# Kernel tuning notes

Measured on AMD Instinct MI355X. Metric: run time of the kernel, lower is better.

The kernel has to match this reference:

```python
import math
import jax, jax.numpy as jnp
import numpy as np

H, DK = 16, 64            # n_heads, d_kv
NUM_BUCKETS, MAX_DIST = 32, 128


def _relative_position_buckets(S):
    # Bidirectional (encoder) T5 bucketization of relative positions.
    ctx = jnp.arange(S, dtype=jnp.int32)[:, None]      # query positions
    mem = jnp.arange(S, dtype=jnp.int32)[None, :]      # key positions
    rp = mem - ctx                                     # [S, S]
    nb = NUM_BUCKETS // 2
    rb = (rp > 0).astype(jnp.int32) * nb
    n = jnp.abs(rp)
    max_exact = nb // 2
    is_small = n < max_exact
    large = max_exact + (
        jnp.log(jnp.maximum(n, 1).astype(jnp.float32) / max_exact)
        / math.log(MAX_DIST / max_exact)
        * (nb - max_exact)
    ).astype(jnp.int32)
    large = jnp.minimum(large, nb - 1)
    return rb + jnp.where(is_small, n, large)          # [S, S] int32


def setup_inputs() -> dict:
    key = jax.random.key(0)
    ks = jax.random.split(key, 6)
    B, S, D = 4, 1024, 1024
    inner = H * DK
    std = 0.02
    return {
        "hidden_states": jax.random.normal(ks[0], (B, S, D), jnp.float32),
        "Wq": jax.random.normal(ks[1], (inner, D), jnp.float32) * std,
        "Wk": jax.random.normal(ks[2], (inner, D), jnp.float32) * std,
        "Wv": jax.random.normal(ks[3], (inner, D), jnp.float32) * std,
        "Wo": jax.random.normal(ks[4], (D, inner), jnp.float32) * std,
        "rel_bias": jax.random.normal(ks[5], (NUM_BUCKETS, H), jnp.float32) * std,
    }


def reference(hidden_states, Wq, Wk, Wv, Wo, rel_bias):
    B, S, D = hidden_states.shape

    def proj(W):  # bias-free linear + split heads -> [B, H, S, DK]
        return (hidden_states @ W.T).reshape(B, S, H, DK).transpose(0, 2, 1, 3)

    q, k, v = proj(Wq), proj(Wk), proj(Wv)
    # T5: NO 1/sqrt(d) scaling
    scores = jnp.einsum("bhqd,bhkd->bhqk", q, k)       # [B, H, S, S]
    bias = rel_bias[_relative_position_buckets(S)]     # [S, S, H]
    scores = scores + bias.transpose(2, 0, 1)[None]    # broadcast over batch
    attn = jax.nn.softmax(scores, axis=-1)
    ctx = jnp.einsum("bhqk,bhkd->bhqd", attn, v)       # [B, H, S, DK]
    ctx = ctx.transpose(0, 2, 1, 3).reshape(B, S, H * DK)
    return ctx @ Wo.T                                  # [B, S, D]
```

## Files before the change

### kernel.cpp

```cpp
#include <hip/hip_runtime.h>

typedef _Float16 half8 __attribute__((ext_vector_type(8)));
typedef _Float16 half4_t __attribute__((ext_vector_type(4)));
typedef float f32x4 __attribute__((ext_vector_type(4)));

#define GK 1024
#define MEG (1024 * 1024)

#define GLD16(gptr, lptr) \
    __builtin_amdgcn_global_load_lds((const __attribute__((address_space(1))) void*)(gptr), \
                                     (__attribute__((address_space(3))) void*)(lptr), 16, 0, 0)

__global__ void cvt_all_kernel(const float* __restrict__ hidden,
                               const float* __restrict__ Wq,
                               const float* __restrict__ Wk,
                               const float* __restrict__ Wv,
                               const float* __restrict__ Wo,
                               _Float16* __restrict__ ws) {
    int b = blockIdx.x;
    const float* src;
    _Float16* dst;
    if (b < 4096)      { src = hidden; dst = ws; }
    else if (b < 5120) { src = Wq; dst = ws + 4 * MEG; b -= 4096; }
    else if (b < 6144) { src = Wk; dst = ws + 5 * MEG; b -= 5120; }
    else if (b < 7168) { src = Wv; dst = ws + 6 * MEG; b -= 6144; }
    else               { src = Wo; dst = ws + 7 * MEG; b -= 7168; }
    int i = (b * 256 + threadIdx.x) * 4;
    f32x4 v = *(const f32x4*)(src + i);
    half4_t h;
    h[0] = (_Float16)v[0]; h[1] = (_Float16)v[1];
    h[2] = (_Float16)v[2]; h[3] = (_Float16)v[3];
    *(half4_t*)(dst + i) = h;
}

template<int MODE>
__global__ __launch_bounds__(256) void gemm_kernel(
    const _Float16* __restrict__ A,
    const _Float16* __restrict__ B0,
    const _Float16* __restrict__ B1,
    const _Float16* __restrict__ B2,
    _Float16* __restrict__ O0,
    _Float16* __restrict__ O1,
    _Float16* __restrict__ O2,
    float* __restrict__ Of)
{
    const _Float16* Bw = B0;
    _Float16* Oh = O0;
    if (MODE == 0) {
        int z = blockIdx.z;
        Bw = (z == 0) ? B0 : ((z == 1) ? B1 : B2);
        Oh = (z == 0) ? O0 : ((z == 1) ? O1 : O2);
    }
    __shared__ __attribute__((aligned(16))) _Float16 sA[128][32];
    __shared__ __attribute__((aligned(16))) _Float16 sB[128][32];

    const int tid = threadIdx.x;
    const int wave = tid >> 6, lane = tid & 63;
    const int quad = lane >> 4, l16 = lane & 15;
    const int wr = wave >> 1, wc = wave & 1;
    const int M0 = blockIdx.y * 128, N0 = blockIdx.x * 128;

    const int rl = lane >> 2;
    const int cl = (lane & 3) * 8;
    const size_t aOff0 = (size_t)(M0 + wave * 16 + rl) * GK + cl;
    const size_t aOff1 = aOff0 + (size_t)64 * GK;
    const size_t bOff0 = (size_t)(N0 + wave * 16 + rl) * GK + cl;
    const size_t bOff1 = bOff0 + (size_t)64 * GK;
    _Float16* ldsA0 = &sA[wave * 16][0];
    _Float16* ldsA1 = &sA[64 + wave * 16][0];
    _Float16* ldsB0 = &sB[wave * 16][0];
    _Float16* ldsB1 = &sB[64 + wave * 16][0];

    f32x4 acc[4][4] = {};

    for (int kt = 0; kt < GK / 32; ++kt) {
        const int ko = kt * 32;
        GLD16(A + aOff0 + ko, ldsA0);
        GLD16(A + aOff1 + ko, ldsA1);
        GLD16(Bw + bOff0 + ko, ldsB0);
        GLD16(Bw + bOff1 + ko, ldsB1);
        __syncthreads();
        half8 af[4], bf[4];
        #pragma unroll
        for (int i = 0; i < 4; ++i)
            af[i] = *(const half8*)&sA[wr * 64 + i * 16 + l16][quad * 8];
        #pragma unroll
        for (int j = 0; j < 4; ++j)
            bf[j] = *(const half8*)&sB[wc * 64 + j * 16 + l16][quad * 8];
        #pragma unroll
        for (int i = 0; i < 4; ++i)
            #pragma unroll
            for (int j = 0; j < 4; ++j)
                acc[i][j] = __builtin_amdgcn_mfma_f32_16x16x32_f16(af[i], bf[j], acc[i][j], 0, 0, 0);
        __syncthreads();
    }

    #pragma unroll
    for (int i = 0; i < 4; ++i) {
        #pragma unroll
        for (int j = 0; j < 4; ++j) {
            #pragma unroll
            for (int r = 0; r < 4; ++r) {
                int m = M0 + wr * 64 + i * 16 + quad * 4 + r;
                int n = N0 + wc * 64 + j * 16 + l16;
                float v = acc[i][j][r];
                if (MODE == 0) {
                    int b = m >> 10, s = m & 1023, hh = n >> 6, d = n & 63;
                    Oh[((size_t)((b * 16 + hh) * 1024 + s)) * 64 + d] = (_Float16)v;
                } else {
                    Of[(size_t)m * 1024 + n] = v;
                }
            }
        }
    }
}

__global__ __launch_bounds__(256) void transpose_v_kernel(
    const _Float16* __restrict__ V, _Float16* __restrict__ VT) {
    __shared__ _Float16 tile[64][65];
    const int s0 = blockIdx.x * 64;
    const int bh = blockIdx.y;
    const _Float16* Vb = V + (size_t)bh * 1024 * 64;
    _Float16* Tb = VT + (size_t)bh * 64 * 1024;
    const int tr = threadIdx.x >> 6;
    const int tc = threadIdx.x & 63;
    #pragma unroll
    for (int i = 0; i < 16; ++i) {
        int r = i * 4 + tr;
        tile[r][tc] = Vb[(size_t)(s0 + r) * 64 + tc];
    }
    __syncthreads();
    #pragma unroll
    for (int i = 0; i < 16; ++i) {
        int d = i * 4 + tr;
        Tb[(size_t)d * 1024 + s0 + tc] = tile[tc][d];
    }
}

__global__ __launch_bounds__(256) void attn_kernel(
    const _Float16* __restrict__ Q,
    const _Float16* __restrict__ K,
    const _Float16* __restrict__ VT,
    const float* __restrict__ rel_bias,
    _Float16* __restrict__ ctx)
{
    const int S = 1024;
    const int q0 = blockIdx.x * 64;
    const int h = blockIdx.y;
    const int b = blockIdx.z;
    const int bh = b * 16 + h;
    const _Float16* Qh = Q + (size_t)bh * S * 64;
    const _Float16* Kh = K + (size_t)bh * S * 64;
    const _Float16* VTh = VT + (size_t)bh * 64 * S;

    __shared__ __attribute__((aligned(16))) _Float16 sQ[64][72];
    __shared__ __attribute__((aligned(16))) _Float16 sK[64][72];
    __shared__ __attribute__((aligned(16))) _Float16 sVt[64][72];
    __shared__ __attribute__((aligned(16))) _Float16 sP[4][16][72];
    __shared__ _Float16 sBias[1088];

    const int tid = threadIdx.x;
    const int wave = tid >> 6, lane = tid & 63;
    const int quad = lane >> 4, l16 = lane & 15;

    {
        int r = tid >> 3, c = (tid & 7) * 8;
        *(half8*)&sQ[r][c]      = *(const half8*)(Qh + (size_t)(q0 + r) * 64 + c);
        *(half8*)&sQ[r + 32][c] = *(const half8*)(Qh + (size_t)(q0 + r + 32) * 64 + c);
    }
    for (int i = tid; i < 1087; i += 256) {
        int delta = i - (q0 + 63);
        int rb = (delta > 0) ? 16 : 0;
        int n = (delta < 0) ? -delta : delta;
        int bucket;
        if (n < 8) bucket = rb + n;
        else bucket = rb + 8 + (n >= 12) + (n >= 16) + (n >= 23) + (n >= 32)
                             + (n >= 46) + (n >= 64) + (n >= 91);
        sBias[i] = (_Float16)rel_bias[bucket * 16 + h];
    }
    __syncthreads();

    half8 qf0 = *(const half8*)&sQ[wave * 16 + l16][quad * 8];
    half8 qf1 = *(const half8*)&sQ[wave * 16 + l16][32 + quad * 8];

    float m_run = -INFINITY, l_run = 0.0f;
    f32x4 acc[4] = {};

    for (int kt = 0; kt < 16; ++kt) {
        __syncthreads();
        {
            int r = tid >> 3, c = (tid & 7) * 8;
            *(half8*)&sK[r][c]      = *(const half8*)(Kh + (size_t)(kt * 64 + r) * 64 + c);
            *(half8*)&sK[r + 32][c] = *(const half8*)(Kh + (size_t)(kt * 64 + r + 32) * 64 + c);
            *(half8*)&sVt[r][c]      = *(const half8*)(VTh + (size_t)r * S + kt * 64 + c);
            *(half8*)&sVt[r + 32][c] = *(const half8*)(VTh + (size_t)(r + 32) * S + kt * 64 + c);
        }
        __syncthreads();

        f32x4 sc[4] = {};
        #pragma unroll
        for (int j = 0; j < 4; ++j) {
            half8 kf0 = *(const half8*)&sK[j * 16 + l16][quad * 8];
            half8 kf1 = *(const half8*)&sK[j * 16 + l16][32 + quad * 8];
            sc[j] = __builtin_amdgcn_mfma_f32_16x16x32_f16(kf0, qf0, sc[j], 0, 0, 0);
            sc[j] = __builtin_amdgcn_mfma_f32_16x16x32_f16(kf1, qf1, sc[j], 0, 0, 0);
        }

        const int bbase = kt * 64 + quad * 4 - wave * 16 - l16 + 63;
        #pragma unroll
        for (int j = 0; j < 4; ++j)
            #pragma unroll
            for (int r = 0; r < 4; ++r)
                sc[j][r] += (float)sBias[bbase + j * 16 + r];

        float mx = fmaxf(fmaxf(fmaxf(sc[0][0], sc[0][1]), fmaxf(sc[0][2], sc[0][3])),
                         fmaxf(fmaxf(sc[1][0], sc[1][1]), fmaxf(sc[1][2], sc[1][3])));
        mx = fmaxf(mx, fmaxf(fmaxf(fmaxf(sc[2][0], sc[2][1]), fmaxf(sc[2][2], sc[2][3])),
                             fmaxf(fmaxf(sc[3][0], sc[3][1]), fmaxf(sc[3][2], sc[3][3]))));
        mx = fmaxf(mx, __shfl_xor(mx, 16));
        mx = fmaxf(mx, __shfl_xor(mx, 32));
        float mnew = fmaxf(m_run, mx);
        float alpha = __expf(m_run - mnew);
        m_run = mnew;

        float ps = 0.0f;
        #pragma unroll
        for (int j = 0; j < 4; ++j) {
            half4_t pw;
            #pragma unroll
            for (int r = 0; r < 4; ++r) {
                float p = __expf(sc[j][r] - mnew);
                ps += p;
                pw[r] = (_Float16)p;
            }
            *(half4_t*)&sP[wave][l16][j * 16 + quad * 4] = pw;
        }
        l_run = l_run * alpha + ps;
        #pragma unroll
        for (int dt = 0; dt < 4; ++dt) acc[dt] *= alpha;
        __syncthreads();

        half8 pf0 = *(const half8*)&sP[wave][l16][quad * 8];
        half8 pf1 = *(const half8*)&sP[wave][l16][32 + quad * 8];
        #pragma unroll
        for (int dt = 0; dt < 4; ++dt) {
            half8 vf0 = *(const half8*)&sVt[dt * 16 + l16][quad * 8];
            half8 vf1 = *(const half8*)&sVt[dt * 16 + l16][32 + quad * 8];
            acc[dt] = __builtin_amdgcn_mfma_f32_16x16x32_f16(vf0, pf0, acc[dt], 0, 0, 0);
            acc[dt] = __builtin_amdgcn_mfma_f32_16x16x32_f16(vf1, pf1, acc[dt], 0, 0, 0);
        }
    }

    l_run += __shfl_xor(l_run, 16);
    l_run += __shfl_xor(l_run, 32);
    const float inv = 1.0f / l_run;
    const size_t qg = (size_t)(b * 1024 + q0 + wave * 16 + l16);
    #pragma unroll
    for (int dt = 0; dt < 4; ++dt) {
        half4_t o;
        #pragma unroll
        for (int r = 0; r < 4; ++r) o[r] = (_Float16)(acc[dt][r] * inv);
        *(half4_t*)&ctx[qg * 1024 + h * 64 + dt * 16 + quad * 4] = o;
    }
}

extern "C" void kernel_launch(void* const* d_in, const int* in_sizes, int n_in,
                              void* d_out, int out_size, void* d_ws, size_t ws_size,
                              hipStream_t stream) {
    const float* hidden   = (const float*)d_in[0];
    const float* Wq       = (const float*)d_in[1];
    const float* Wk       = (const float*)d_in[2];
    const float* Wv       = (const float*)d_in[3];
    const float* Wo       = (const float*)d_in[4];
    const float* rel_bias = (const float*)d_in[5];
    float* out = (float*)d_out;

    _Float16* ws    = (_Float16*)d_ws;
    _Float16* h16   = ws;
    _Float16* wq16  = ws + 4 * (size_t)MEG;
    _Float16* wk16  = ws + 5 * (size_t)MEG;
    _Float16* wv16  = ws + 6 * (size_t)MEG;
    _Float16* wo16  = ws + 7 * (size_t)MEG;
    _Float16* Qs    = ws + 8 * (size_t)MEG;
    _Float16* Ks    = ws + 12 * (size_t)MEG;
    _Float16* Vs    = ws + 16 * (size_t)MEG;
    _Float16* ctx16 = ws + 20 * (size_t)MEG;
    _Float16* VTs   = h16;

    cvt_all_kernel<<<8192, 256, 0, stream>>>(hidden, Wq, Wk, Wv, Wo, ws);

    gemm_kernel<0><<<dim3(8, 32, 3), 256, 0, stream>>>(
        h16, wq16, wk16, wv16, Qs, Ks, Vs, nullptr);

    transpose_v_kernel<<<dim3(16, 64), 256, 0, stream>>>(Vs, VTs);

    attn_kernel<<<dim3(16, 16, 4), 256, 0, stream>>>(Qs, Ks, VTs, rel_bias, ctx16);

    gemm_kernel<1><<<dim3(8, 32, 1), 256, 0, stream>>>(
        ctx16, wo16, nullptr, nullptr, nullptr, nullptr, nullptr, out);
}
```

Measured before the change: 217.9 us.

## Widen GEMM K-step to 64 and use constant bias for far attention tiles

The GEMM main loop now loads two 32-wide K chunks into separate LDS buffers per iteration, which halves the number of barrier pairs and issues more MFMAs between syncs. The attention kernel uses the fact that T5 relative-position buckets saturate beyond distance 128. For key tiles at least three tiles away from the query tile it adds a single bias value instead of sixteen LDS lookups. This uses more LDS in the GEMM and adds a branch in attention. The bias shortcut holds only because the bucket is constant at those distances.

```diff
diff --git a/kernel.cpp b/kernel.cpp
--- a/kernel.cpp
+++ b/kernel.cpp
@@ -51,8 +51,8 @@
         Bw = (z == 0) ? B0 : ((z == 1) ? B1 : B2);
         Oh = (z == 0) ? O0 : ((z == 1) ? O1 : O2);
     }
-    __shared__ __attribute__((aligned(16))) _Float16 sA[128][32];
-    __shared__ __attribute__((aligned(16))) _Float16 sB[128][32];
+    __shared__ __attribute__((aligned(16))) _Float16 sA[2][128][32];
+    __shared__ __attribute__((aligned(16))) _Float16 sB[2][128][32];
 
     const int tid = threadIdx.x;
     const int wave = tid >> 6, lane = tid & 63;
@@ -62,36 +62,42 @@
 
     const int rl = lane >> 2;
     const int cl = (lane & 3) * 8;
-    const size_t aOff0 = (size_t)(M0 + wave * 16 + rl) * GK + cl;
-    const size_t aOff1 = aOff0 + (size_t)64 * GK;
-    const size_t bOff0 = (size_t)(N0 + wave * 16 + rl) * GK + cl;
-    const size_t bOff1 = bOff0 + (size_t)64 * GK;
-    _Float16* ldsA0 = &sA[wave * 16][0];
-    _Float16* ldsA1 = &sA[64 + wave * 16][0];
-    _Float16* ldsB0 = &sB[wave * 16][0];
-    _Float16* ldsB1 = &sB[64 + wave * 16][0];
+    const size_t aRow0 = (size_t)(M0 + wave * 16 + rl) * GK + cl;
+    const size_t aRow1 = aRow0 + (size_t)64 * GK;
+    const size_t bRow0 = (size_t)(N0 + wave * 16 + rl) * GK + cl;
+    const size_t bRow1 = bRow0 + (size_t)64 * GK;
+    _Float16* ldsA[2][2] = {{&sA[0][wave * 16][0], &sA[0][64 + wave * 16][0]},
+                            {&sA[1][wave * 16][0], &sA[1][64 + wave * 16][0]}};
+    _Float16* ldsB[2][2] = {{&sB[0][wave * 16][0], &sB[0][64 + wave * 16][0]},
+                            {&sB[1][wave * 16][0], &sB[1][64 + wave * 16][0]}};
 
     f32x4 acc[4][4] = {};
 
-    for (int kt = 0; kt < GK / 32; ++kt) {
-        const int ko = kt * 32;
-        GLD16(A + aOff0 + ko, ldsA0);
-        GLD16(A + aOff1 + ko, ldsA1);
-        GLD16(Bw + bOff0 + ko, ldsB0);
-        GLD16(Bw + bOff1 + ko, ldsB1);
-        __syncthreads();
-        half8 af[4], bf[4];
-        #pragma unroll
-        for (int i = 0; i < 4; ++i)
-            af[i] = *(const half8*)&sA[wr * 64 + i * 16 + l16][quad * 8];
-        #pragma unroll
-        for (int j = 0; j < 4; ++j)
-            bf[j] = *(const half8*)&sB[wc * 64 + j * 16 + l16][quad * 8];
-        #pragma unroll
-        for (int i = 0; i < 4; ++i)
+    for (int kt = 0; kt < GK / 64; ++kt) {
+        const int ko = kt * 64;
+        #pragma unroll
+        for (int c = 0; c < 2; ++c) {
+            GLD16(A + aRow0 + ko + c * 32, ldsA[c][0]);
+            GLD16(A + aRow1 + ko + c * 32, ldsA[c][1]);
+            GLD16(Bw + bRow0 + ko + c * 32, ldsB[c][0]);
+            GLD16(Bw + bRow1 + ko + c * 32, ldsB[c][1]);
+        }
+        __syncthreads();
+        #pragma unroll
+        for (int c = 0; c < 2; ++c) {
+            half8 af[4], bf[4];
+            #pragma unroll
+            for (int i = 0; i < 4; ++i)
+                af[i] = *(const half8*)&sA[c][wr * 64 + i * 16 + l16][quad * 8];
             #pragma unroll
             for (int j = 0; j < 4; ++j)
-                acc[i][j] = __builtin_amdgcn_mfma_f32_16x16x32_f16(af[i], bf[j], acc[i][j], 0, 0, 0);
+                bf[j] = *(const half8*)&sB[c][wc * 64 + j * 16 + l16][quad * 8];
+            #pragma unroll
+            for (int i = 0; i < 4; ++i)
+                #pragma unroll
+                for (int j = 0; j < 4; ++j)
+                    acc[i][j] = __builtin_amdgcn_mfma_f32_16x16x32_f16(af[i], bf[j], acc[i][j], 0, 0, 0);
+        }
         __syncthreads();
     }
 
@@ -145,7 +151,8 @@
     _Float16* __restrict__ ctx)
 {
     const int S = 1024;
-    const int q0 = blockIdx.x * 64;
+    const int qt = blockIdx.x;
+    const int q0 = qt * 64;
     const int h = blockIdx.y;
     const int b = blockIdx.z;
     const int bh = b * 16 + h;
@@ -207,11 +214,20 @@
         }
 
         const int bbase = kt * 64 + quad * 4 - wave * 16 - l16 + 63;
-        #pragma unroll
-        for (int j = 0; j < 4; ++j)
-            #pragma unroll
-            for (int r = 0; r < 4; ++r)
-                sc[j][r] += (float)sBias[bbase + j * 16 + r];
+        if (kt <= qt - 3 || kt >= qt + 3) {
+            const float cb = (float)sBias[bbase];
+            #pragma unroll
+            for (int j = 0; j < 4; ++j)
+                #pragma unroll
+                for (int r = 0; r < 4; ++r)
+                    sc[j][r] += cb;
+        } else {
+            #pragma unroll
+            for (int j = 0; j < 4; ++j)
+                #pragma unroll
+                for (int r = 0; r < 4; ++r)
+                    sc[j][r] += (float)sBias[bbase + j * 16 + r];
+        }
 
         float mx = fmaxf(fmaxf(fmaxf(sc[0][0], sc[0][1]), fmaxf(sc[0][2], sc[0][3])),
                          fmaxf(fmaxf(sc[1][0], sc[1][1]), fmaxf(sc[1][2], sc[1][3])));
```

Result: faster. 206.7 us (-5.1%).
